# Optimization experiments

Measured on AMD Instinct MI355X. Metric: run time of the kernel, lower is better.

Reference implementation:

```python
import jax, jax.numpy as jnp
import numpy as np

L, D, H, IMG, P, B, E = 12, 768, 12, 224, 16, 32, 512
HD = D // H            # 64
FF = 4 * D             # 3072
SEQ = (IMG // P) ** 2 + 1  # 197


def _ln(x, w, b, eps=1e-5):
    m = x.mean(-1, keepdims=True)
    v = jnp.mean((x - m) ** 2, axis=-1, keepdims=True)
    return (x - m) * jax.lax.rsqrt(v + eps) * w + b


def setup_inputs() -> dict:
    key = jax.random.key(0)
    ks = jax.random.split(key, 10)
    r = lambda k, shape, s=0.02: (jax.random.normal(k, shape, jnp.float32) * s)
    return {
        'image': jax.random.normal(ks[0], (B, 3, IMG, IMG), jnp.float32),
        'conv_w': r(ks[1], (D, 3, P, P)),
        'cls_emb': r(ks[2], (D,)),
        'pos_emb': r(ks[3], (SEQ, D)),
        'ln_pre_w': jnp.ones((D,), jnp.float32), 'ln_pre_b': jnp.zeros((D,), jnp.float32),
        'ln1_w': jnp.ones((L, D), jnp.float32), 'ln1_b': jnp.zeros((L, D), jnp.float32),
        'qkv_w': r(ks[4], (L, 3 * D, D)), 'qkv_b': jnp.zeros((L, 3 * D), jnp.float32),
        'out_w': r(ks[5], (L, D, D)), 'out_b': jnp.zeros((L, D), jnp.float32),
        'ln2_w': jnp.ones((L, D), jnp.float32), 'ln2_b': jnp.zeros((L, D), jnp.float32),
        'fc_w': r(ks[6], (L, FF, D)), 'fc_b': jnp.zeros((L, FF), jnp.float32),
        'pr_w': r(ks[7], (L, D, FF)), 'pr_b': jnp.zeros((L, D), jnp.float32),
        'ln_post_w': jnp.ones((D,), jnp.float32), 'ln_post_b': jnp.zeros((D,), jnp.float32),
        'proj': r(ks[8], (D, E)),
    }


def reference(image, conv_w, cls_emb, pos_emb, ln_pre_w, ln_pre_b,
              ln1_w, ln1_b, qkv_w, qkv_b, out_w, out_b,
              ln2_w, ln2_b, fc_w, fc_b, pr_w, pr_b,
              ln_post_w, ln_post_b, proj):
    # patchify: conv stride=kernel=patch, no bias -> [B, D, 14, 14]
    x = jax.lax.conv_general_dilated(image, conv_w, (P, P), 'VALID',
                                     dimension_numbers=('NCHW', 'OIHW', 'NCHW'))
    x = x.reshape(B, D, -1).transpose(0, 2, 1)               # [B, 196, D]
    cls = jnp.broadcast_to(cls_emb, (B, 1, D))
    x = jnp.concatenate([cls, x], axis=1) + pos_emb          # [B, SEQ, D]
    x = _ln(x, ln_pre_w, ln_pre_b)
    x = x.transpose(1, 0, 2)                                  # [SEQ, B, D]
    scale = 1.0 / np.sqrt(HD).astype(np.float32)

    def step(x, p):
        l1w, l1b, qw, qb, ow, ob, l2w, l2b, fw, fb, pw, pb = p
        h = _ln(x, l1w, l1b)
        qkv = h @ qw.T + qb                                    # [SEQ, B, 3D]
        q, k, v = jnp.split(qkv, 3, axis=-1)
        heads = lambda t: t.reshape(SEQ, B * H, HD).transpose(1, 0, 2)  # [B*H, SEQ, HD]
        q = heads(q) * scale
        k = heads(k)
        v = heads(v)
        a = jax.nn.softmax(jnp.einsum('nsh,nth->nst', q, k), axis=-1)   # [B*H, SEQ, SEQ]
        o = jnp.einsum('nst,nth->nsh', a, v)                  # [B*H, SEQ, HD]
        o = o.transpose(1, 0, 2).reshape(SEQ, B, D)
        x = x + (o @ ow.T + ob)
        h = _ln(x, l2w, l2b)
        h = jax.nn.gelu(h @ fw.T + fb, approximate=False)      # torch nn.GELU (exact)
        x = x + (h @ pw.T + pb)
        return x, None

    x, _ = jax.lax.scan(step, x, (ln1_w, ln1_b, qkv_w, qkv_b, out_w, out_b,
                                  ln2_w, ln2_b, fc_w, fc_b, pr_w, pr_b))
    x = x.transpose(1, 0, 2)                                   # [B, SEQ, D]
    cls_tok = _ln(x[:, 0, :], ln_post_w, ln_post_b)
    feats = cls_tok @ proj                                     # [B, E]
    return feats / jnp.linalg.norm(feats, axis=-1, keepdims=True)
```

## Files before the change

kernel.cpp:

```cpp
#include <hip/hip_runtime.h>
#include <stdint.h>

#define SEQ 197
#define NB 32
#define NH 12
#define NTOK (SEQ*NB)
#define MPAD 6400
#define NPATCH 6272

typedef unsigned short u16;
typedef unsigned int u32;
typedef __attribute__((ext_vector_type(8))) short bv8;
typedef __attribute__((ext_vector_type(4))) float f32x4;

__device__ __forceinline__ u16 f2bf(float f){
  u32 u = __float_as_uint(f);
  u = (u + 0x7fffu + ((u >> 16) & 1u)) >> 16;
  return (u16)u;
}
__device__ __forceinline__ float bf2f(u16 h){ return __uint_as_float(((u32)h) << 16); }

#if defined(__has_builtin)
#if __has_builtin(__builtin_amdgcn_global_load_lds)
#define HAS_GLLDS 1
#endif
#endif

__device__ __forceinline__ void gl_lds16(const void* g, void* l){
#ifdef HAS_GLLDS
  __builtin_amdgcn_global_load_lds(
      (const __attribute__((address_space(1))) void*)(uintptr_t)g,
      (__attribute__((address_space(3))) void*)(u32)(uintptr_t)l, 16, 0, 0);
#else
  int lane = threadIdx.x & 63;
  uint4 v = *(const uint4*)((const char*)g);
  *(uint4*)((char*)l + lane*16) = v;
#endif
}

__device__ __forceinline__ void red2(float& a, float& b){
  #pragma unroll
  for (int o = 32; o > 0; o >>= 1){ a += __shfl_down(a, o); b += __shfl_down(b, o); }
  __shared__ float red[8];
  int w = threadIdx.x >> 6, ln = threadIdx.x & 63;
  if (ln == 0){ red[w] = a; red[4 + w] = b; }
  __syncthreads();
  a = red[0] + red[1] + red[2] + red[3];
  b = red[4] + red[5] + red[6] + red[7];
}

__global__ __launch_bounds__(256) void cvt_k(const float* __restrict__ src, u16* __restrict__ dst, int n4){
  int i = blockIdx.x * 256 + threadIdx.x;
  if (i >= n4) return;
  float4 f = ((const float4*)src)[i];
  u32 lo = (u32)f2bf(f.x) | ((u32)f2bf(f.y) << 16);
  u32 hi = (u32)f2bf(f.z) | ((u32)f2bf(f.w) << 16);
  ((uint2*)dst)[i] = make_uint2(lo, hi);
}

__global__ __launch_bounds__(256) void im2col_k(const float* __restrict__ img, u16* __restrict__ Ap){
  int gid = blockIdx.x * 256 + threadIdx.x;
  int row = gid / 768, k = gid - row * 768;
  int b = row / 196, p = row - b * 196;
  int pr = p / 14, pc = p - pr * 14;
  int c = k >> 8, r = k & 255;
  int ph = r >> 4, pw = r & 15;
  size_t src = ((size_t)(b * 3 + c) * 224 + (pr * 16 + ph)) * 224 + (pc * 16 + pw);
  Ap[gid] = f2bf(img[src]);
}

template<int EPI>
__global__ __launch_bounds__(256, 2)
void gemm_sw(const u16* __restrict__ A, const u16* __restrict__ Bw,
             const float* __restrict__ bias, float* __restrict__ Cf,
             u16* __restrict__ Cb, int N, int K, int Mreal,
             int RM, int RN, int tmT, int tnT)
{
  __shared__ __align__(16) u16 sA[128 * 64];
  __shared__ __align__(16) u16 sB[128 * 64];
  const int xcd = blockIdx.x & 7, pos = blockIdx.x >> 3;
  const int xm = xcd >> 1, xn = xcd & 1;
  const int tm = xm * RM + pos / RN;
  const int tn = xn * RN + pos % RN;
  if (tm >= tmT || tn >= tnT) return;

  const int tid = threadIdx.x;
  const int lane = tid & 63, wave = tid >> 6;
  const int wm = wave >> 1, wn = wave & 1;
  const int lr = lane & 15, g = lane >> 4, g4 = g * 4;
  const int KT = K >> 6;

  const int srow = lane >> 3;
  const int sch = (lane & 7) ^ srow;
  const u16* aB[4]; const u16* bB[4];
  u16* lA[4]; u16* lB[4];
  #pragma unroll
  for (int j = 0; j < 4; j++){
    int rr = wave * 32 + j * 8;
    aB[j] = A  + (size_t)(tm * 128 + rr + srow) * K + sch * 8;
    bB[j] = Bw + (size_t)(tn * 128 + rr + srow) * K + sch * 8;
    lA[j] = sA + rr * 64;
    lB[j] = sB + rr * 64;
  }

  f32x4 acc[4][4] = {};

  for (int kt = 0; kt < KT; ++kt){
    __syncthreads();
    #pragma unroll
    for (int j = 0; j < 4; j++) gl_lds16(aB[j] + (size_t)kt * 64, lA[j]);
    #pragma unroll
    for (int j = 0; j < 4; j++) gl_lds16(bB[j] + (size_t)kt * 64, lB[j]);
    __syncthreads();
    #pragma unroll
    for (int kk = 0; kk < 2; kk++){
      bv8 af[4], bf[4];
      #pragma unroll
      for (int mi = 0; mi < 4; mi++){
        int row = wm * 64 + mi * 16 + lr;
        af[mi] = *(const bv8*)((const char*)sA + row * 128 + ((kk * 64 + g * 16) ^ ((row & 7) << 4)));
      }
      #pragma unroll
      for (int ni = 0; ni < 4; ni++){
        int row = wn * 64 + ni * 16 + lr;
        bf[ni] = *(const bv8*)((const char*)sB + row * 128 + ((kk * 64 + g * 16) ^ ((row & 7) << 4)));
      }
      #pragma unroll
      for (int mi = 0; mi < 4; mi++)
        #pragma unroll
        for (int ni = 0; ni < 4; ni++)
          acc[mi][ni] = __builtin_amdgcn_mfma_f32_16x16x32_bf16(af[mi], bf[ni], acc[mi][ni], 0, 0, 0);
    }
  }

  if (EPI == 1 || EPI == 3){
    __syncthreads();
    u16* sC = sA;
    #pragma unroll
    for (int mi = 0; mi < 4; mi++){
      #pragma unroll
      for (int ni = 0; ni < 4; ni++){
        int bcol = wn * 64 + ni * 16 + lr;
        float bvs = bias[tn * 128 + bcol];
        #pragma unroll
        for (int j = 0; j < 4; j++){
          int brow = wm * 64 + mi * 16 + g4 + j;
          float v = acc[mi][ni][j] + bvs;
          if (EPI == 3) v = 0.5f * v * (1.f + erff(v * 0.70710678118654752f));
          *(u16*)((char*)sC + brow * 256 + ((bcol * 2) ^ ((brow & 7) << 4))) = f2bf(v);
        }
      }
    }
    __syncthreads();
    #pragma unroll
    for (int c = 0; c < 8; c++){
      int off = c * 4096 + tid * 16;
      int row = off >> 8;
      int colb = off & 255;
      uint4 v = *(const uint4*)((const char*)sC + row * 256 + (colb ^ ((row & 7) << 4)));
      *(uint4*)((char*)(Cb + (size_t)(tm * 128 + row) * N + tn * 128) + colb) = v;
    }
  } else {
    #pragma unroll
    for (int ni = 0; ni < 4; ni++){
      int col = tn * 128 + wn * 64 + ni * 16 + lr;
      float bvs = (EPI != 0) ? bias[col] : 0.f;
      #pragma unroll
      for (int mi = 0; mi < 4; mi++){
        int row0 = tm * 128 + wm * 64 + mi * 16 + g4;
        #pragma unroll
        for (int j = 0; j < 4; j++){
          int row = row0 + j;
          if (row < Mreal){
            float v = acc[mi][ni][j] + bvs;
            size_t idx = (size_t)row * N + col;
            if (EPI == 0) Cf[idx] = v;
            else          Cf[idx] += v;
          }
        }
      }
    }
  }
}

template<int EPI>
__global__ __launch_bounds__(256, 2)
void gemm_2ph(const u16* __restrict__ A, const u16* __restrict__ Bw,
              const float* __restrict__ bias, float* __restrict__ Cf,
              u16* __restrict__ Cb, int N, int K, int Mreal,
              int RM, int RN, int tmT, int tnT)
{
  __shared__ __align__(16) u16 sA0[128 * 64];
  __shared__ __align__(16) u16 sB0[128 * 64];
  __shared__ __align__(16) u16 sA1[128 * 64];
  __shared__ __align__(16) u16 sB1[128 * 64];
  const int xcd = blockIdx.x & 7, pos = blockIdx.x >> 3;
  const int xm = xcd >> 1, xn = xcd & 1;
  const int tm = xm * RM + pos / RN;
  const int tn = xn * RN + pos % RN;
  if (tm >= tmT || tn >= tnT) return;

  const int tid = threadIdx.x;
  const int lane = tid & 63, wave = tid >> 6;
  const int wm = wave >> 1, wn = wave & 1;
  const int lr = lane & 15, g = lane >> 4, g4 = g * 4;
  const int KT = K >> 6;

  const int srow = lane >> 3;
  const int sch = (lane & 7) ^ srow;
  const u16* aB[4]; const u16* bB[4];
  #pragma unroll
  for (int j = 0; j < 4; j++){
    int rr = wave * 32 + j * 8;
    aB[j] = A  + (size_t)(tm * 128 + rr + srow) * K + sch * 8;
    bB[j] = Bw + (size_t)(tn * 128 + rr + srow) * K + sch * 8;
  }

  f32x4 acc[4][4] = {};

  auto stage = [&](int kt, u16* dA, u16* dB){
    #pragma unroll
    for (int j = 0; j < 4; j++)
      gl_lds16(aB[j] + (size_t)kt * 64, dA + (wave * 32 + j * 8) * 64);
    #pragma unroll
    for (int j = 0; j < 4; j++)
      gl_lds16(bB[j] + (size_t)kt * 64, dB + (wave * 32 + j * 8) * 64);
  };
  auto tile = [&](const u16* sA, const u16* sB, u16* dA, u16* dB, int ktNext, bool doStage, bool last){
    if (last) asm volatile("s_waitcnt vmcnt(0)" ::: "memory");
    else      asm volatile("s_waitcnt vmcnt(8)" ::: "memory");
    __builtin_amdgcn_s_barrier();
    bv8 af[4][2], bf[4][2];
    #pragma unroll
    for (int mi = 0; mi < 4; mi++){
      int row = wm * 64 + mi * 16 + lr;
      #pragma unroll
      for (int kk = 0; kk < 2; kk++)
        af[mi][kk] = *(const bv8*)((const char*)sA + row * 128 + ((kk * 64 + g * 16) ^ ((row & 7) << 4)));
    }
    #pragma unroll
    for (int ni = 0; ni < 4; ni++){
      int row = wn * 64 + ni * 16 + lr;
      #pragma unroll
      for (int kk = 0; kk < 2; kk++)
        bf[ni][kk] = *(const bv8*)((const char*)sB + row * 128 + ((kk * 64 + g * 16) ^ ((row & 7) << 4)));
    }
    asm volatile("s_waitcnt lgkmcnt(0)" ::: "memory");
    __builtin_amdgcn_s_barrier();
    if (doStage) stage(ktNext, dA, dB);
    __builtin_amdgcn_s_setprio(1);
    #pragma unroll
    for (int kk = 0; kk < 2; kk++)
      #pragma unroll
      for (int mi = 0; mi < 4; mi++)
        #pragma unroll
        for (int ni = 0; ni < 4; ni++)
          acc[mi][ni] = __builtin_amdgcn_mfma_f32_16x16x32_bf16(af[mi][kk], bf[ni][kk], acc[mi][ni], 0, 0, 0);
    __builtin_amdgcn_s_setprio(0);
  };

  stage(0, sA0, sB0);
  stage(1, sA1, sB1);
  int t = 0;
  for (; t + 2 < KT; t += 2){
    tile(sA0, sB0, sA0, sB0, t + 2, true,  false);
    tile(sA1, sB1, sA1, sB1, t + 3, true,  false);
  }
  tile(sA0, sB0, sA0, sB0, 0, false, false);
  tile(sA1, sB1, sA1, sB1, 0, false, true);

  #pragma unroll
  for (int ni = 0; ni < 4; ni++){
    int col = tn * 128 + wn * 64 + ni * 16 + lr;
    float bvs = (EPI != 0) ? bias[col] : 0.f;
    #pragma unroll
    for (int mi = 0; mi < 4; mi++){
      int row0 = tm * 128 + wm * 64 + mi * 16 + g4;
      #pragma unroll
      for (int j = 0; j < 4; j++){
        int row = row0 + j;
        if (row < Mreal){
          float v = acc[mi][ni][j] + bvs;
          size_t idx = (size_t)row * N + col;
          if (EPI == 0) Cf[idx] = v;
          else          Cf[idx] += v;
        }
      }
    }
  }
}

__global__ __launch_bounds__(256, 2) void attn_k(const u16* __restrict__ qkv, u16* __restrict__ o_out){
  __shared__ __align__(16) u16 sK[256 * 64];
  __shared__ __align__(16) u16 sVT[64 * 256];
  __shared__ __align__(16) u16 sP[4 * 32 * 64];
  const int bh2 = blockIdx.x;
  const int bh = bh2 >> 1, half = bh2 & 1;
  const int b = bh / NH, h = bh - b * NH;
  const int tid = threadIdx.x;
  const int lane = tid & 63, wave = tid >> 6;
  const int lr = lane & 15, g = lane >> 4;
  const int g4 = g * 4;
  const int wb = half * 128 + wave * 32;
  const u16* kbase = qkv + (size_t)b * SEQ * 2304 + h * 64 + 768;
  const u16* vbase = kbase + 768;

  bv8 qf[2][2];
  #pragma unroll
  for (int qt = 0; qt < 2; qt++){
    int q = wb + qt * 16 + lr; if (q > 196) q = 196;
    const u16* qr = qkv + (size_t)(b * SEQ + q) * 2304 + h * 64;
    #pragma unroll
    for (int kc = 0; kc < 2; kc++)
      qf[qt][kc] = *(const bv8*)(qr + kc * 32 + g * 8);
  }

  for (int i = tid; i < 197 * 32; i += 256){
    int r = i >> 5, c = i & 31;
    u32 kv_ = *(const u32*)(kbase + (size_t)r * 2304 + c * 2);
    *(u32*)((char*)sK + ((r * 128 + c * 4) ^ ((r & 7) << 4))) = kv_;
    u32 vv = *(const u32*)(vbase + (size_t)r * 2304 + c * 2);
    int hd0 = c * 2, hd1 = c * 2 + 1;
    *(u16*)((char*)sVT + ((hd0 * 512 + r * 2) ^ ((hd0 & 7) << 4))) = (u16)(vv & 0xffff);
    *(u16*)((char*)sVT + ((hd1 * 512 + r * 2) ^ ((hd1 & 7) << 4))) = (u16)(vv >> 16);
  }
  for (int i = tid; i < 59 * 32; i += 256){
    int r = 197 + (i >> 5), c = i & 31;
    *(u32*)((char*)sK + (r * 128 + c * 4)) = 0;
  }
  for (int i = tid; i < 59 * 64; i += 256){
    int kv = 197 + (i >> 6), hd = i & 63;
    *(u16*)((char*)sVT + ((hd * 512 + kv * 2) ^ ((hd & 7) << 4))) = 0;
  }
  __syncthreads();

  f32x4 acc_o[2][4] = {};
  float m_[2] = {-1e30f, -1e30f};
  float l_[2] = {0.f, 0.f};
  u16* sPw = sP + wave * 2048;

  for (int ch = 0; ch < 4; ++ch){
    f32x4 st[4][2] = {};
    #pragma unroll
    for (int kc = 0; kc < 2; kc++){
      bv8 kf[4];
      #pragma unroll
      for (int kvt = 0; kvt < 4; kvt++){
        int row = ch * 64 + kvt * 16 + lr;
        kf[kvt] = *(const bv8*)((const char*)sK + ((row * 128 + kc * 64 + g * 16) ^ ((row & 7) << 4)));
      }
      #pragma unroll
      for (int kvt = 0; kvt < 4; kvt++)
        #pragma unroll
        for (int qt = 0; qt < 2; qt++)
          st[kvt][qt] = __builtin_amdgcn_mfma_f32_16x16x32_bf16(kf[kvt], qf[qt][kc], st[kvt][qt], 0, 0, 0);
    }
    float fac[2];
    #pragma unroll
    for (int qt = 0; qt < 2; qt++){
      float mx = -1e30f;
      #pragma unroll
      for (int kvt = 0; kvt < 4; kvt++)
        #pragma unroll
        for (int j = 0; j < 4; j++){
          int kvg = ch * 64 + kvt * 16 + g4 + j;
          float s = st[kvt][qt][j] * 0.125f;
          s = (kvg < 197) ? s : -1e30f;
          st[kvt][qt][j] = s;
          mx = fmaxf(mx, s);
        }
      mx = fmaxf(mx, __shfl_xor(mx, 16));
      mx = fmaxf(mx, __shfl_xor(mx, 32));
      float nm = fmaxf(m_[qt], mx);
      fac[qt] = __expf(m_[qt] - nm);
      m_[qt] = nm;
      float ls = 0.f;
      #pragma unroll
      for (int kvt = 0; kvt < 4; kvt++)
        #pragma unroll
        for (int j = 0; j < 4; j++){
          float p = __expf(st[kvt][qt][j] - nm);
          st[kvt][qt][j] = p;
          ls += p;
        }
      ls += __shfl_xor(ls, 16);
      ls += __shfl_xor(ls, 32);
      l_[qt] = l_[qt] * fac[qt] + ls;
    }
    #pragma unroll
    for (int qt = 0; qt < 2; qt++)
      #pragma unroll
      for (int j = 0; j < 4; j++){
        float fj = __shfl(fac[qt], (lane & 48) | (g4 + j));
        #pragma unroll
        for (int nt = 0; nt < 4; nt++) acc_o[qt][nt][j] *= fj;
      }
    #pragma unroll
    for (int qt = 0; qt < 2; qt++){
      int row = qt * 16 + lr;
      #pragma unroll
      for (int kvt = 0; kvt < 4; kvt++){
        uint2 pk;
        pk.x = (u32)f2bf(st[kvt][qt][0]) | ((u32)f2bf(st[kvt][qt][1]) << 16);
        pk.y = (u32)f2bf(st[kvt][qt][2]) | ((u32)f2bf(st[kvt][qt][3]) << 16);
        *(uint2*)((char*)sPw + ((row * 128 + kvt * 32 + g * 8) ^ ((row & 7) << 4))) = pk;
      }
    }
    #pragma unroll
    for (int kc = 0; kc < 2; kc++){
      bv8 pa[2], vb[4];
      #pragma unroll
      for (int qt = 0; qt < 2; qt++){
        int row = qt * 16 + lr;
        pa[qt] = *(const bv8*)((const char*)sPw + ((row * 128 + kc * 64 + g * 16) ^ ((row & 7) << 4)));
      }
      #pragma unroll
      for (int nt = 0; nt < 4; nt++){
        int hd = nt * 16 + lr;
        vb[nt] = *(const bv8*)((const char*)sVT + ((hd * 512 + ch * 128 + kc * 64 + g * 16) ^ ((hd & 7) << 4)));
      }
      #pragma unroll
      for (int qt = 0; qt < 2; qt++)
        #pragma unroll
        for (int nt = 0; nt < 4; nt++)
          acc_o[qt][nt] = __builtin_amdgcn_mfma_f32_16x16x32_bf16(pa[qt], vb[nt], acc_o[qt][nt], 0, 0, 0);
    }
  }

  #pragma unroll
  for (int qt = 0; qt < 2; qt++)
    #pragma unroll
    for (int j = 0; j < 4; j++){
      float lj = __shfl(l_[qt], (lane & 48) | (g4 + j));
      float rl = 1.f / lj;
      int row = wb + qt * 16 + g4 + j;
      if (row < 197){
        u16* dst = o_out + (size_t)(b * SEQ + row) * 768 + h * 64;
        #pragma unroll
        for (int nt = 0; nt < 4; nt++)
          dst[nt * 16 + lr] = f2bf(acc_o[qt][nt][j] * rl);
      }
    }
}

__global__ __launch_bounds__(256) void embed_ln_k(const float* __restrict__ patch, const float* __restrict__ cls,
    const float* __restrict__ pos, const float* __restrict__ w, const float* __restrict__ bb, float* __restrict__ x)
{
  int t = blockIdx.x;
  int b = t / SEQ, s = t - b * SEQ;
  int tid = threadIdx.x;
  float v[3];
  #pragma unroll
  for (int i = 0; i < 3; i++){
    int d = tid + i * 256;
    float base = (s == 0) ? cls[d] : patch[(size_t)(b * 196 + s - 1) * 768 + d];
    v[i] = base + pos[s * 768 + d];
  }
  float sm = v[0] + v[1] + v[2];
  float sq = v[0]*v[0] + v[1]*v[1] + v[2]*v[2];
  red2(sm, sq);
  float m = sm * (1.f / 768.f);
  float rs = rsqrtf(sq * (1.f / 768.f) - m * m + 1e-5f);
  #pragma unroll
  for (int i = 0; i < 3; i++){
    int d = tid + i * 256;
    x[(size_t)t * 768 + d] = (v[i] - m) * rs * w[d] + bb[d];
  }
}

__global__ __launch_bounds__(256) void ln_bf16_k(const float* __restrict__ x, const float* __restrict__ w,
    const float* __restrict__ bb, u16* __restrict__ h)
{
  int t = blockIdx.x, tid = threadIdx.x;
  const float* xr = x + (size_t)t * 768;
  float v[3];
  #pragma unroll
  for (int i = 0; i < 3; i++) v[i] = xr[tid + i * 256];
  float sm = v[0] + v[1] + v[2];
  float sq = v[0]*v[0] + v[1]*v[1] + v[2]*v[2];
  red2(sm, sq);
  float m = sm * (1.f / 768.f);
  float rs = rsqrtf(sq * (1.f / 768.f) - m * m + 1e-5f);
  #pragma unroll
  for (int i = 0; i < 3; i++){
    int d = tid + i * 256;
    h[(size_t)t * 768 + d] = f2bf((v[i] - m) * rs * w[d] + bb[d]);
  }
}

__global__ __launch_bounds__(256) void ln_cls_k(const float* __restrict__ x, const float* __restrict__ w,
    const float* __restrict__ bb, float* __restrict__ cls)
{
  int b = blockIdx.x, tid = threadIdx.x;
  const float* xr = x + (size_t)b * SEQ * 768;
  float v[3];
  #pragma unroll
  for (int i = 0; i < 3; i++) v[i] = xr[tid + i * 256];
  float sm = v[0] + v[1] + v[2];
  float sq = v[0]*v[0] + v[1]*v[1] + v[2]*v[2];
  red2(sm, sq);
  float m = sm * (1.f / 768.f);
  float rs = rsqrtf(sq * (1.f / 768.f) - m * m + 1e-5f);
  #pragma unroll
  for (int i = 0; i < 3; i++){
    int d = tid + i * 256;
    cls[b * 768 + d] = (v[i] - m) * rs * w[d] + bb[d];
  }
}

__global__ __launch_bounds__(256) void proj_k(const float* __restrict__ cls, const float* __restrict__ P,
                                              float* __restrict__ feats){
  int gid = blockIdx.x * 256 + threadIdx.x;
  int b = gid >> 9, e = gid & 511;
  const float* c = cls + b * 768;
  float a0 = 0, a1 = 0, a2 = 0, a3 = 0;
  for (int d = 0; d < 768; d += 4){
    a0 += c[d]     * P[(size_t)d * 512 + e];
    a1 += c[d + 1] * P[(size_t)(d + 1) * 512 + e];
    a2 += c[d + 2] * P[(size_t)(d + 2) * 512 + e];
    a3 += c[d + 3] * P[(size_t)(d + 3) * 512 + e];
  }
  feats[gid] = (a0 + a1) + (a2 + a3);
}

__global__ __launch_bounds__(256) void norm_k(const float* __restrict__ feats, float* __restrict__ out){
  int b = blockIdx.x, tid = threadIdx.x;
  float v0 = feats[b * 512 + tid], v1 = feats[b * 512 + 256 + tid];
  float sq = v0 * v0 + v1 * v1, dummy = 0.f;
  red2(sq, dummy);
  float inv = 1.f / sqrtf(sq);
  out[b * 512 + tid] = v0 * inv;
  out[b * 512 + 256 + tid] = v1 * inv;
}

extern "C" void kernel_launch(void* const* d_in, const int* in_sizes, int n_in,
                              void* d_out, int out_size, void* d_ws, size_t ws_size,
                              hipStream_t stream)
{
  const float* image   = (const float*)d_in[0];
  const float* conv_w  = (const float*)d_in[1];
  const float* cls_emb = (const float*)d_in[2];
  const float* pos_emb = (const float*)d_in[3];
  const float* lnprew  = (const float*)d_in[4];
  const float* lnpreb  = (const float*)d_in[5];
  const float* ln1w    = (const float*)d_in[6];
  const float* ln1b    = (const float*)d_in[7];
  const float* qkvw    = (const float*)d_in[8];
  const float* qkvb    = (const float*)d_in[9];
  const float* outw    = (const float*)d_in[10];
  const float* outb    = (const float*)d_in[11];
  const float* ln2w    = (const float*)d_in[12];
  const float* ln2b    = (const float*)d_in[13];
  const float* fcw     = (const float*)d_in[14];
  const float* fcb     = (const float*)d_in[15];
  const float* prw     = (const float*)d_in[16];
  const float* prb     = (const float*)d_in[17];
  const float* lnpostw = (const float*)d_in[18];
  const float* lnpostb = (const float*)d_in[19];
  const float* proj    = (const float*)d_in[20];
  (void)in_sizes; (void)n_in; (void)out_size;

  const size_t QW = (size_t)2304 * 768, OW = (size_t)768 * 768;
  const size_t FW = (size_t)3072 * 768, PW = (size_t)768 * 3072;
  const size_t CW = (size_t)768 * 768;

  char* p = (char*)d_ws;
  auto alloc = [&](size_t bytes)->char*{ char* r = p; p += (bytes + 255) & ~(size_t)255; return r; };
  float* x     = (float*)alloc((size_t)MPAD * 768 * 4);
  u16*   h     = (u16*)  alloc((size_t)MPAD * 768 * 2);
  u16*   qkvB  = (u16*)  alloc((size_t)MPAD * 2304 * 2);
  u16*   attno = (u16*)  alloc((size_t)MPAD * 768 * 2);
  u16*   ffh   = (u16*)  alloc((size_t)MPAD * 3072 * 2);
  u16*   Ap    = (u16*)  alloc((size_t)NPATCH * 768 * 2);
  float* patch = (float*)alloc((size_t)NPATCH * 768 * 4);
  float* clsb  = (float*)alloc((size_t)32 * 768 * 4);
  float* feats = (float*)alloc((size_t)32 * 512 * 4);
  u16*   cwb   = (u16*)  alloc(CW * 2);
  size_t base_used = (size_t)(p - (char*)d_ws);
  size_t full_need = (QW + OW + FW + PW) * 12 * 2;
  bool full = (base_used + full_need + 4096 <= ws_size);

  u16 *wq = nullptr, *wo = nullptr, *wf = nullptr, *wp = nullptr;
  u16 *sq_ = nullptr, *so_ = nullptr, *sf_ = nullptr, *sp_ = nullptr;
  if (full){
    wq = (u16*)alloc(QW * 12 * 2); wo = (u16*)alloc(OW * 12 * 2);
    wf = (u16*)alloc(FW * 12 * 2); wp = (u16*)alloc(PW * 12 * 2);
  } else {
    sq_ = (u16*)alloc(QW * 2); so_ = (u16*)alloc(OW * 2);
    sf_ = (u16*)alloc(FW * 2); sp_ = (u16*)alloc(PW * 2);
  }
  if ((size_t)(p - (char*)d_ws) > ws_size) return;

  { int n4 = (int)(CW / 4); cvt_k<<<(n4 + 255) / 256, 256, 0, stream>>>(conv_w, cwb, n4); }
  if (full){
    int n4;
    n4 = (int)(QW * 12 / 4); cvt_k<<<(n4 + 255) / 256, 256, 0, stream>>>(qkvw, wq, n4);
    n4 = (int)(OW * 12 / 4); cvt_k<<<(n4 + 255) / 256, 256, 0, stream>>>(outw, wo, n4);
    n4 = (int)(FW * 12 / 4); cvt_k<<<(n4 + 255) / 256, 256, 0, stream>>>(fcw,  wf, n4);
    n4 = (int)(PW * 12 / 4); cvt_k<<<(n4 + 255) / 256, 256, 0, stream>>>(prw,  wp, n4);
  }

  im2col_k<<<(NPATCH * 768) / 256, 256, 0, stream>>>(image, Ap);
  gemm_sw<0><<<8 * 13 * 3, 256, 0, stream>>>(Ap, cwb, nullptr, patch, nullptr, 768, 768, NPATCH, 13, 3, 49, 6);
  embed_ln_k<<<NTOK, 256, 0, stream>>>(patch, cls_emb, pos_emb, lnprew, lnpreb, x);

  for (int l = 0; l < 12; l++){
    const u16 *WQ, *WO, *WF, *WP;
    if (full){
      WQ = wq + (size_t)l * QW; WO = wo + (size_t)l * OW;
      WF = wf + (size_t)l * FW; WP = wp + (size_t)l * PW;
    } else {
      int n4;
      n4 = (int)(QW / 4); cvt_k<<<(n4 + 255) / 256, 256, 0, stream>>>(qkvw + (size_t)l * QW, sq_, n4);
      n4 = (int)(OW / 4); cvt_k<<<(n4 + 255) / 256, 256, 0, stream>>>(outw + (size_t)l * OW, so_, n4);
      n4 = (int)(FW / 4); cvt_k<<<(n4 + 255) / 256, 256, 0, stream>>>(fcw  + (size_t)l * FW, sf_, n4);
      n4 = (int)(PW / 4); cvt_k<<<(n4 + 255) / 256, 256, 0, stream>>>(prw  + (size_t)l * PW, sp_, n4);
      WQ = sq_; WO = so_; WF = sf_; WP = sp_;
    }
    ln_bf16_k<<<NTOK, 256, 0, stream>>>(x, ln1w + l * 768, ln1b + l * 768, h);
    gemm_sw<1><<<8 * 13 * 9, 256, 0, stream>>>(h, WQ, qkvb + l * 2304, nullptr, qkvB, 2304, 768, NTOK, 13, 9, 50, 18);
    attn_k<<<NB * NH * 2, 256, 0, stream>>>(qkvB, attno);
    gemm_sw<2><<<8 * 13 * 3, 256, 0, stream>>>(attno, WO, outb + l * 768, x, nullptr, 768, 768, NTOK, 13, 3, 50, 6);
    ln_bf16_k<<<NTOK, 256, 0, stream>>>(x, ln2w + l * 768, ln2b + l * 768, h);
    gemm_sw<3><<<8 * 13 * 12, 256, 0, stream>>>(h, WF, fcb + l * 3072, nullptr, ffh, 3072, 768, NTOK, 13, 12, 50, 24);
    gemm_2ph<2><<<8 * 13 * 3, 256, 0, stream>>>(ffh, WP, prb + l * 768, x, nullptr, 768, 3072, NTOK, 13, 3, 50, 6);
  }

  ln_cls_k<<<NB, 256, 0, stream>>>(x, lnpostw, lnpostb, clsb);
  proj_k<<<(NB * 512) / 256, 256, 0, stream>>>(clsb, proj, feats);
  norm_k<<<NB, 256, 0, stream>>>(feats, (float*)d_out);
}
```

Measured before the change: 2.735 ms.

## Split-K the out-proj and FFN down-proj GEMMs with atomic accumulation

Adds a split-K dimension via blockIdx.y to gemm_sw and gemm_2ph. The out-projection and FFN-down residual GEMMs now launch two K-halves that accumulate into x with float atomics, and only the first split adds the bias. The N=768 GEMMs only had 300 tiles, so the goal is more blocks per launch and better CU occupancy. In exchange it adds atomic traffic and makes the fp32 summation order nondeterministic.

```diff
diff --git a/kernel.cpp b/kernel.cpp
--- a/kernel.cpp
+++ b/kernel.cpp
@@ -73,7 +73,7 @@
 __global__ __launch_bounds__(256, 2)
 void gemm_sw(const u16* __restrict__ A, const u16* __restrict__ Bw,
              const float* __restrict__ bias, float* __restrict__ Cf,
-             u16* __restrict__ Cb, int N, int K, int Mreal,
+             u16* __restrict__ Cb, int N, int Kst, int kLen, int Mreal,
              int RM, int RN, int tmT, int tnT)
 {
   __shared__ __align__(16) u16 sA[128 * 64];
@@ -83,12 +83,14 @@
   const int tm = xm * RM + pos / RN;
   const int tn = xn * RN + pos % RN;
   if (tm >= tmT || tn >= tnT) return;
+  const int kOff = blockIdx.y * kLen;
+  const bool addB = (EPI != 0) && (blockIdx.y == 0);
 
   const int tid = threadIdx.x;
   const int lane = tid & 63, wave = tid >> 6;
   const int wm = wave >> 1, wn = wave & 1;
   const int lr = lane & 15, g = lane >> 4, g4 = g * 4;
-  const int KT = K >> 6;
+  const int KT = kLen >> 6;
 
   const int srow = lane >> 3;
   const int sch = (lane & 7) ^ srow;
@@ -97,8 +99,8 @@
   #pragma unroll
   for (int j = 0; j < 4; j++){
     int rr = wave * 32 + j * 8;
-    aB[j] = A  + (size_t)(tm * 128 + rr + srow) * K + sch * 8;
-    bB[j] = Bw + (size_t)(tn * 128 + rr + srow) * K + sch * 8;
+    aB[j] = A  + (size_t)(tm * 128 + rr + srow) * Kst + kOff + sch * 8;
+    bB[j] = Bw + (size_t)(tn * 128 + rr + srow) * Kst + kOff + sch * 8;
     lA[j] = sA + rr * 64;
     lB[j] = sB + rr * 64;
   }
@@ -164,7 +166,7 @@
     #pragma unroll
     for (int ni = 0; ni < 4; ni++){
       int col = tn * 128 + wn * 64 + ni * 16 + lr;
-      float bvs = (EPI != 0) ? bias[col] : 0.f;
+      float bvs = addB ? bias[col] : 0.f;
       #pragma unroll
       for (int mi = 0; mi < 4; mi++){
         int row0 = tm * 128 + wm * 64 + mi * 16 + g4;
@@ -175,7 +177,7 @@
             float v = acc[mi][ni][j] + bvs;
             size_t idx = (size_t)row * N + col;
             if (EPI == 0) Cf[idx] = v;
-            else          Cf[idx] += v;
+            else          unsafeAtomicAdd(&Cf[idx], v);
           }
         }
       }
@@ -187,7 +189,7 @@
 __global__ __launch_bounds__(256, 2)
 void gemm_2ph(const u16* __restrict__ A, const u16* __restrict__ Bw,
               const float* __restrict__ bias, float* __restrict__ Cf,
-              u16* __restrict__ Cb, int N, int K, int Mreal,
+              int N, int Kst, int kLen, int Mreal,
               int RM, int RN, int tmT, int tnT)
 {
   __shared__ __align__(16) u16 sA0[128 * 64];
@@ -199,12 +201,14 @@
   const int tm = xm * RM + pos / RN;
   const int tn = xn * RN + pos % RN;
   if (tm >= tmT || tn >= tnT) return;
+  const int kOff = blockIdx.y * kLen;
+  const bool addB = (blockIdx.y == 0);
 
   const int tid = threadIdx.x;
   const int lane = tid & 63, wave = tid >> 6;
   const int wm = wave >> 1, wn = wave & 1;
   const int lr = lane & 15, g = lane >> 4, g4 = g * 4;
-  const int KT = K >> 6;
+  const int KT = kLen >> 6;
 
   const int srow = lane >> 3;
   const int sch = (lane & 7) ^ srow;
@@ -212,8 +216,8 @@
   #pragma unroll
   for (int j = 0; j < 4; j++){
     int rr = wave * 32 + j * 8;
-    aB[j] = A  + (size_t)(tm * 128 + rr + srow) * K + sch * 8;
-    bB[j] = Bw + (size_t)(tn * 128 + rr + srow) * K + sch * 8;
+    aB[j] = A  + (size_t)(tm * 128 + rr + srow) * Kst + kOff + sch * 8;
+    bB[j] = Bw + (size_t)(tn * 128 + rr + srow) * Kst + kOff + sch * 8;
   }
 
   f32x4 acc[4][4] = {};
@@ -272,7 +276,7 @@
   #pragma unroll
   for (int ni = 0; ni < 4; ni++){
     int col = tn * 128 + wn * 64 + ni * 16 + lr;
-    float bvs = (EPI != 0) ? bias[col] : 0.f;
+    float bvs = addB ? bias[col] : 0.f;
     #pragma unroll
     for (int mi = 0; mi < 4; mi++){
       int row0 = tm * 128 + wm * 64 + mi * 16 + g4;
@@ -281,9 +285,7 @@
         int row = row0 + j;
         if (row < Mreal){
           float v = acc[mi][ni][j] + bvs;
-          size_t idx = (size_t)row * N + col;
-          if (EPI == 0) Cf[idx] = v;
-          else          Cf[idx] += v;
+          unsafeAtomicAdd(&Cf[(size_t)row * N + col], v);
         }
       }
     }
@@ -601,7 +603,7 @@
   }
 
   im2col_k<<<(NPATCH * 768) / 256, 256, 0, stream>>>(image, Ap);
-  gemm_sw<0><<<8 * 13 * 3, 256, 0, stream>>>(Ap, cwb, nullptr, patch, nullptr, 768, 768, NPATCH, 13, 3, 49, 6);
+  gemm_sw<0><<<8 * 13 * 3, 256, 0, stream>>>(Ap, cwb, nullptr, patch, nullptr, 768, 768, 768, NPATCH, 13, 3, 49, 6);
   embed_ln_k<<<NTOK, 256, 0, stream>>>(patch, cls_emb, pos_emb, lnprew, lnpreb, x);
 
   for (int l = 0; l < 12; l++){
@@ -618,12 +620,12 @@
       WQ = sq_; WO = so_; WF = sf_; WP = sp_;
     }
     ln_bf16_k<<<NTOK, 256, 0, stream>>>(x, ln1w + l * 768, ln1b + l * 768, h);
-    gemm_sw<1><<<8 * 13 * 9, 256, 0, stream>>>(h, WQ, qkvb + l * 2304, nullptr, qkvB, 2304, 768, NTOK, 13, 9, 50, 18);
+    gemm_sw<1><<<8 * 13 * 9, 256, 0, stream>>>(h, WQ, qkvb + l * 2304, nullptr, qkvB, 2304, 768, 768, NTOK, 13, 9, 50, 18);
     attn_k<<<NB * NH * 2, 256, 0, stream>>>(qkvB, attno);
-    gemm_sw<2><<<8 * 13 * 3, 256, 0, stream>>>(attno, WO, outb + l * 768, x, nullptr, 768, 768, NTOK, 13, 3, 50, 6);
+    gemm_sw<2><<<dim3(8 * 13 * 3, 2), 256, 0, stream>>>(attno, WO, outb + l * 768, x, nullptr, 768, 768, 384, NTOK, 13, 3, 50, 6);
     ln_bf16_k<<<NTOK, 256, 0, stream>>>(x, ln2w + l * 768, ln2b + l * 768, h);
-    gemm_sw<3><<<8 * 13 * 12, 256, 0, stream>>>(h, WF, fcb + l * 3072, nullptr, ffh, 3072, 768, NTOK, 13, 12, 50, 24);
-    gemm_2ph<2><<<8 * 13 * 3, 256, 0, stream>>>(ffh, WP, prb + l * 768, x, nullptr, 768, 3072, NTOK, 13, 3, 50, 6);
+    gemm_sw<3><<<8 * 13 * 12, 256, 0, stream>>>(h, WF, fcb + l * 3072, nullptr, ffh, 3072, 768, 768, NTOK, 13, 12, 50, 24);
+    gemm_2ph<2><<<dim3(8 * 13 * 3, 2), 256, 0, stream>>>(ffh, WP, prb + l * 768, x, 768, 3072, 1536, NTOK, 13, 3, 50, 6);
   }
 
   ln_cls_k<<<NB, 256, 0, stream>>>(x, lnpostw, lnpostb, clsb);
```

New measurement: 3.126 ms. 14.3% more time.
